# Optimization experiments

Measured on AMD Instinct MI355X. Metric: run time of the kernel, lower is better.

Reference implementation:

```python
import jax, jax.numpy as jnp
import numpy as np
import math

PC_MIN_X, PC_MIN_Y = 0.0, -40.0
VOXEL = 0.05
STRIDE = 8
PE_CH = 16
NEG_SLOPE = 0.01
BN_EPS = 1e-5


def _grid_points():
    # get_pseudo_points: centers of stride-8 BEV cells
    xs = np.arange(0.2, 70.4, 0.4, dtype=np.float32)    # 176
    ys = np.arange(-39.8, 40.2, 0.4, dtype=np.float32)  # 200
    gx, gy = np.meshgrid(xs, ys)                        # (200, 176)
    return jnp.asarray(np.stack([gx, gy], -1).reshape(-1, 2))  # [P, 2]


def _pe3d(D, H, W):
    ch = PE_CH
    div = jnp.exp(jnp.arange(0, ch, 2, dtype=jnp.float32) * (-math.log(10000.0) / ch))
    def enc(n):
        t = jnp.arange(n, dtype=jnp.float32)[:, None] * div[None, :]
        return jnp.concatenate([jnp.sin(t), jnp.cos(t)], axis=-1)  # [n, ch]
    pex = jnp.broadcast_to(enc(D)[:, None, None, :], (D, H, W, ch))
    pey = jnp.broadcast_to(enc(H)[None, :, None, :], (D, H, W, ch))
    pez = jnp.broadcast_to(enc(W)[None, None, :, :], (D, H, W, ch))
    return jnp.concatenate([pex, pey, pez], axis=-1).transpose(3, 0, 1, 2)  # [3*ch, D, H, W]


def _bn_lrelu(h, g, b):
    # eval-mode BatchNorm3d with running_mean=0, running_var=1, then LeakyReLU(0.01)
    h = h * (g / np.sqrt(1.0 + BN_EPS))[None, :, None, None, None] + b[None, :, None, None, None]
    return jnp.where(h >= 0, h, NEG_SLOPE * h)


def _dvf(x, w1, b1, g1, be1, w2, b2, g2, be2, w3, b3):
    N, C, D, H, W = x.shape
    pe = _pe3d(D, H, W)  # [48, D, H, W]
    feats = jnp.concatenate([x, jnp.broadcast_to(pe[None], (N,) + pe.shape)], axis=1)
    h = jnp.einsum('ncdhw,oc->nodhw', feats, w1) + b1[None, :, None, None, None]
    h = _bn_lrelu(h, g1, be1)
    h = jnp.einsum('ncdhw,oc->nodhw', h, w2) + b2[None, :, None, None, None]
    h = _bn_lrelu(h, g2, be2)
    logits = jnp.einsum('ncdhw,oc->nodhw', h, w3) + b3[None, :, None, None, None]  # [N,1,D,H,W]
    wts = jax.nn.softmax(logits, axis=2)  # softmax over depth D
    return (x * wts).reshape(N, C * D, H, W)


def _bilinear(im, x, y):
    # im: (H, W, C), x/y: (P,)  -- faithful to bilinear_interpolate_torch
    H, W = im.shape[0], im.shape[1]
    xf = jnp.floor(x).astype(jnp.int32)
    yf = jnp.floor(y).astype(jnp.int32)
    x0 = jnp.clip(xf, 0, W - 1)
    x1 = jnp.clip(xf + 1, 0, W - 1)
    y0 = jnp.clip(yf, 0, H - 1)
    y1 = jnp.clip(yf + 1, 0, H - 1)
    Ia, Ib, Ic, Id = im[y0, x0], im[y1, x0], im[y0, x1], im[y1, x1]
    x0f, x1f = x0.astype(x.dtype), x1.astype(x.dtype)
    y0f, y1f = y0.astype(y.dtype), y1.astype(y.dtype)
    wa = (x1f - x) * (y1f - y)
    wb = (x1f - x) * (y - y0f)
    wc = (x - x0f) * (y1f - y)
    wd = (x - x0f) * (y - y0f)
    return Ia * wa[:, None] + Ib * wb[:, None] + Ic * wc[:, None] + Id * wd[:, None]


def _rot(p, theta):
    c, s = jnp.cos(theta), jnp.sin(theta)
    return jnp.stack([p[:, 0] * c - p[:, 1] * s, p[:, 0] * s + p[:, 1] * c], axis=-1)


def _bev_align_one(feat, th_prev, th_cur, grid):
    # feat: [C', H, W]; X_TRANS modeled as z-rotation: fwd(current) then inverse(previous)
    Hh, Ww = feat.shape[1], feat.shape[2]
    p = _rot(grid, th_cur)
    p = _rot(p, -th_prev)
    xi = (p[:, 0] - PC_MIN_X) / VOXEL / STRIDE
    yi = (p[:, 1] - PC_MIN_Y) / VOXEL / STRIDE
    out = _bilinear(feat.transpose(1, 2, 0), xi, yi)  # [P, C']
    return out.reshape(Hh, Ww, -1).transpose(2, 0, 1)


def setup_inputs() -> dict:
    key = jax.random.key(0)
    ks = jax.random.split(key, 16)
    N, C, D, H, W = 4, 64, 2, 200, 176
    IN1 = PE_CH * 3 + C  # 112
    inp = {
        'x0': jax.random.normal(ks[0], (N, C, D, H, W), jnp.float32),
        'x1': jax.random.normal(ks[1], (N, C, D, H, W), jnp.float32),
        'transform_param': jax.random.normal(ks[2], (N, 2), jnp.float32) * 0.3,
        'w1': jax.random.normal(ks[3], (C, IN1), jnp.float32) * 0.05,
        'b1': jax.random.normal(ks[4], (C,), jnp.float32) * 0.05,
        'g1': jax.random.uniform(ks[5], (C,), jnp.float32, 0.5, 1.5),
        'be1': jax.random.normal(ks[6], (C,), jnp.float32) * 0.05,
        'w2': jax.random.normal(ks[7], (C // 2, C), jnp.float32) * 0.05,
        'b2': jax.random.normal(ks[8], (C // 2,), jnp.float32) * 0.05,
        'g2': jax.random.uniform(ks[9], (C // 2,), jnp.float32, 0.5, 1.5),
        'be2': jax.random.normal(ks[10], (C // 2,), jnp.float32) * 0.05,
        'w3': jax.random.normal(ks[11], (1, C // 2), jnp.float32) * 0.05,
        'b3': jax.random.normal(ks[12], (1,), jnp.float32) * 0.05,
    }
    return inp


def reference(x0, x1, transform_param, w1, b1, g1, be1, w2, b2, g2, be2, w3, b3):
    mlp = (w1, b1, g1, be1, w2, b2, g2, be2, w3, b3)
    f0 = _dvf(x0, *mlp)  # rot 0: [N, C*D, H, W]
    f1 = _dvf(x1, *mlp)  # rot 1
    grid = _grid_points()
    aligned = jax.vmap(lambda f, tp: _bev_align_one(f, tp[0], tp[1], grid))(f1, transform_param)
    return jnp.maximum(f0, aligned)  # ALIGN_METHOD='max' over stacked feats
```

## Files before the change

kernel.cpp:

```cpp
#include <hip/hip_runtime.h>
#include <hip/hip_bf16.h>
#include <cmath>

#define HW   35200
#define CD   128

typedef short bf16x8 __attribute__((ext_vector_type(8)));
typedef float f32x4  __attribute__((ext_vector_type(4)));

union Frag { unsigned u[4]; bf16x8 v; };

#define OFF_W1B   0
#define OFF_W2B   3072
#define OFF_TD    4096
#define OFF_B2F   4224
#define OFF_W3F   4256
#define OFF_PE    4288
#define OFF_F0B   567488
#define OFF_F1B   9578688

__device__ __forceinline__ float lrelu(float v) { return v >= 0.f ? v : 0.01f * v; }
__device__ __forceinline__ unsigned short f2bf(float f) {
  union { __hip_bfloat16 h; unsigned short u; } c;
  c.h = __float2bfloat16(f);
  return c.u;
}
__device__ __forceinline__ unsigned pack2bf(float lo, float hi) {
  union { __hip_bfloat162 h2; unsigned u; } c;
  c.h2 = __float22bfloat162_rn(float2{lo, hi});
  return c.u;
}
__device__ __forceinline__ float bflo(unsigned u) { return __uint_as_float(u << 16); }
__device__ __forceinline__ float bfhi(unsigned u) { return __uint_as_float(u & 0xffff0000u); }

__global__ void setup_kernel(const float* __restrict__ w1, const float* __restrict__ b1,
                             const float* __restrict__ g1, const float* __restrict__ be1,
                             const float* __restrict__ w2, const float* __restrict__ b2,
                             const float* __restrict__ g2, const float* __restrict__ be2,
                             const float* __restrict__ w3, const float* __restrict__ b3,
                             float* __restrict__ ws) {
  const float RS = rsqrtf(1.0f + 1e-5f);
  unsigned short* w1b = (unsigned short*)(ws + OFF_W1B);
  unsigned short* w2b = (unsigned short*)(ws + OFF_W2B);
  unsigned short* pe  = (unsigned short*)(ws + OFF_PE);
  int i = blockIdx.x * blockDim.x + threadIdx.x;
  if (i < 6144) {
    int e = i & 7, l = (i >> 3) & 63, nt = (i >> 9) & 3, kh = i >> 11;
    int n = nt * 16 + (l & 15);
    int k = kh * 32 + (l >> 4) * 8 + e;
    int col = (kh < 2) ? k : (80 + (k - 64));
    w1b[i] = f2bf(w1[n * 112 + col] * (g1[n] * RS));
    return;
  }
  i -= 6144;
  if (i < 2048) {
    int e = i & 7, l = (i >> 3) & 63, nt = (i >> 9) & 1, kh = i >> 10;
    int n = nt * 16 + (l & 15);
    int k = kh * 32 + (l >> 4) * 8 + e;
    w2b[i] = f2bf(w2[n * 64 + k] * (g2[n] * RS));
    return;
  }
  i -= 2048;
  if (i < 128) {
    int d = i >> 6, o = i & 63;
    float a = 0.f;
    for (int j = 0; j < 8; ++j) {
      float dv = expf((float)(2 * j) * (-0.5756462732485115f));
      float t  = (float)d * dv;
      a += w1[o * 112 + 64 + j] * sinf(t) + w1[o * 112 + 72 + j] * cosf(t);
    }
    ws[OFF_TD + d * 64 + o] = (g1[o] * RS) * (b1[o] + a) + be1[o];
    return;
  }
  i -= 128;
  if (i < 32) { ws[OFF_B2F + i] = b2[i] * (g2[i] * RS) + be2[i]; return; }
  i -= 32;
  if (i < 32) { ws[OFF_W3F + i] = w3[i]; return; }
  i -= 32;
  if (i < 563200) {
    int hw = i >> 4, j = i & 15;
    int h = hw / 176, w = hw - h * 176;
    int jj = j & 7;
    float dv = expf((float)(2 * jj) * (-0.5756462732485115f));
    if (j < 8) {
      float t = (float)h * dv;
      pe[hw * 32 + jj]      = f2bf(sinf(t));
      pe[hw * 32 + 8 + jj]  = f2bf(cosf(t));
    } else {
      float t = (float)w * dv;
      pe[hw * 32 + 16 + jj] = f2bf(sinf(t));
      pe[hw * 32 + 24 + jj] = f2bf(cosf(t));
    }
  }
}

__global__ __launch_bounds__(256)
void mlp_kernel(const float* __restrict__ x0, const float* __restrict__ x1,
                const float* __restrict__ wtab,
                unsigned short* __restrict__ f0b, unsigned short* __restrict__ f1b) {
  __shared__ alignas(16) unsigned short Hs[8 * 128 * 8];

  const int t    = threadIdx.x;
  const int lane = t & 63;
  const int wv   = __builtin_amdgcn_readfirstlane(t >> 6);
  const int g    = lane >> 4;
  const int li   = lane & 15;
  const int n    = blockIdx.y;
  const int inp  = blockIdx.z;
  const int hw0  = blockIdx.x * 64;
  const int pxs  = wv * 16 + li;
  const float* xn = (inp ? x1 : x0) + (size_t)n * CD * HW;
  unsigned short* dst = inp ? f1b : f0b;
  const unsigned short* w1bu = (const unsigned short*)(wtab + OFF_W1B);
  const unsigned short* w2bu = (const unsigned short*)(wtab + OFF_W2B);
  const unsigned short* peg  = (const unsigned short*)(wtab + OFF_PE);

  float xf[2][2][8];
#pragma unroll
  for (int ti = 0; ti < 2; ++ti)
#pragma unroll
    for (int kh = 0; kh < 2; ++kh)
#pragma unroll
      for (int e = 0; e < 8; ++e) {
        const int c = kh * 32 + g * 8 + e;
        xf[ti][kh][e] = xn[(size_t)(c * 2 + ti) * HW + hw0 + pxs];
      }
  const uint4 pev = *(const uint4*)(peg + (size_t)(hw0 + pxs) * 32 + g * 8);

  Frag xb[2][2];
#pragma unroll
  for (int ti = 0; ti < 2; ++ti)
#pragma unroll
    for (int kh = 0; kh < 2; ++kh)
#pragma unroll
      for (int q = 0; q < 4; ++q)
        xb[ti][kh].u[q] = pack2bf(xf[ti][kh][2 * q], xf[ti][kh][2 * q + 1]);
  Frag pf;
  pf.u[0] = pev.x; pf.u[1] = pev.y; pf.u[2] = pev.z; pf.u[3] = pev.w;

  f32x4 acc[2][4];
#pragma unroll
  for (int ti = 0; ti < 2; ++ti)
#pragma unroll
    for (int nt = 0; nt < 4; ++nt) {
      const float tdv = wtab[OFF_TD + ti * 64 + nt * 16 + li];
      acc[ti][nt] = (f32x4){tdv, tdv, tdv, tdv};
    }
#pragma unroll
  for (int kh = 0; kh < 2; ++kh)
#pragma unroll
    for (int nt = 0; nt < 4; ++nt) {
      const bf16x8 b = *(const bf16x8*)&w1bu[(unsigned)((kh * 4 + nt) * 64 + lane) * 8];
      acc[0][nt] = __builtin_amdgcn_mfma_f32_16x16x32_bf16(xb[0][kh].v, b, acc[0][nt], 0, 0, 0);
      acc[1][nt] = __builtin_amdgcn_mfma_f32_16x16x32_bf16(xb[1][kh].v, b, acc[1][nt], 0, 0, 0);
    }
#pragma unroll
  for (int nt = 0; nt < 4; ++nt) {
    const bf16x8 b = *(const bf16x8*)&w1bu[(unsigned)((8 + nt) * 64 + lane) * 8];
    acc[0][nt] = __builtin_amdgcn_mfma_f32_16x16x32_bf16(pf.v, b, acc[0][nt], 0, 0, 0);
    acc[1][nt] = __builtin_amdgcn_mfma_f32_16x16x32_bf16(pf.v, b, acc[1][nt], 0, 0, 0);
  }

#pragma unroll
  for (int ti = 0; ti < 2; ++ti) {
    const int tau = wv + ti * 4;
#pragma unroll
    for (int nt = 0; nt < 4; ++nt)
#pragma unroll
      for (int r = 0; r < 4; ++r) {
        const int o   = nt * 16 + li;
        const int row = tau * 16 + g * 4 + r;
        Hs[(unsigned)((o >> 3) * 128 + row) * 8 + (o & 7)] = f2bf(lrelu(acc[ti][nt][r]));
      }
  }

  f32x4 acc2[2][2];
#pragma unroll
  for (int nt = 0; nt < 2; ++nt) {
    const float bv = wtab[OFF_B2F + nt * 16 + li];
    acc2[0][nt] = (f32x4){bv, bv, bv, bv};
    acc2[1][nt] = acc2[0][nt];
  }
#pragma unroll
  for (int kh = 0; kh < 2; ++kh) {
    const bf16x8 a0 = *(const bf16x8*)&Hs[(unsigned)((kh * 4 + g) * 128 + (wv + 0) * 16 + li) * 8];
    const bf16x8 a1 = *(const bf16x8*)&Hs[(unsigned)((kh * 4 + g) * 128 + (wv + 4) * 16 + li) * 8];
#pragma unroll
    for (int nt = 0; nt < 2; ++nt) {
      const bf16x8 b = *(const bf16x8*)&w2bu[(unsigned)((kh * 2 + nt) * 64 + lane) * 8];
      acc2[0][nt] = __builtin_amdgcn_mfma_f32_16x16x32_bf16(a0, b, acc2[0][nt], 0, 0, 0);
      acc2[1][nt] = __builtin_amdgcn_mfma_f32_16x16x32_bf16(a1, b, acc2[1][nt], 0, 0, 0);
    }
  }

  const float w3a = wtab[OFF_W3F + li];
  const float w3b = wtab[OFF_W3F + 16 + li];
  float wt0[4], wt1[4];
#pragma unroll
  for (int r = 0; r < 4; ++r) {
    float p0 = w3a * lrelu(acc2[0][0][r]) + w3b * lrelu(acc2[0][1][r]);
    float p1 = w3a * lrelu(acc2[1][0][r]) + w3b * lrelu(acc2[1][1][r]);
    p0 += __shfl_xor(p0, 1); p0 += __shfl_xor(p0, 2);
    p0 += __shfl_xor(p0, 4); p0 += __shfl_xor(p0, 8);
    p1 += __shfl_xor(p1, 1); p1 += __shfl_xor(p1, 2);
    p1 += __shfl_xor(p1, 4); p1 += __shfl_xor(p1, 8);
    wt0[r] = 1.f / (1.f + expf(p1 - p0));
    wt1[r] = 1.f / (1.f + expf(p0 - p1));
  }

  const int src = (li >> 2) << 4;
  const float a0 = __shfl(wt0[0], src), b0 = __shfl(wt1[0], src);
  const float a1 = __shfl(wt0[1], src), b1v = __shfl(wt1[1], src);
  const float a2 = __shfl(wt0[2], src), b2v = __shfl(wt1[2], src);
  const float a3 = __shfl(wt0[3], src), b3v = __shfl(wt1[3], src);
  const int r = li & 3;
  const float w0  = (r == 0) ? a0 : (r == 1) ? a1 : (r == 2) ? a2 : a3;
  const float w1v = (r == 0) ? b0 : (r == 1) ? b1v : (r == 2) ? b2v : b3v;

#pragma unroll
  for (int kh = 0; kh < 2; ++kh)
#pragma unroll
    for (int j = 0; j < 4; ++j) {
      const int k = kh * 16 + g * 4 + j;
      const unsigned ua = xb[0][kh].u[j];
      const unsigned ub = xb[1][kh].u[j];
      uint2 pk;
      pk.x = pack2bf(bflo(ua) * w0, bflo(ub) * w1v);
      pk.y = pack2bf(bfhi(ua) * w0, bfhi(ub) * w1v);
      *(uint2*)&dst[(((size_t)n * 32 + k) * HW + hw0 + pxs) * 4] = pk;
    }
}

__global__ __launch_bounds__(256)
void gather_max_kernel(const unsigned short* __restrict__ f0b,
                       const unsigned short* __restrict__ f1b,
                       const float* __restrict__ tp,
                       float* __restrict__ out) {
  const int orig = blockIdx.x;
  const int xcd = orig & 7, idx = orig >> 3;
  const int tile = (xcd < 6 ? xcd * 69 : 6 * 69 + (xcd - 6) * 68) + idx;

  const int tix = threadIdx.x;
  const int px  = tix & 63;
  const int q   = tix >> 6;
  const int n   = blockIdx.y;
  const int hw  = tile * 64 + px;
  const int h   = hw / 176;
  const int w   = hw - h * 176;

  const float thp = tp[n * 2 + 0], thc = tp[n * 2 + 1];
  const float gx = 0.2f + 0.4f * (float)w;
  const float gy = -39.8f + 0.4f * (float)h;
  const float c1 = cosf(thc),  s1v = sinf(thc);
  const float p1x = gx * c1 - gy * s1v;
  const float p1y = gx * s1v + gy * c1;
  const float c2 = cosf(-thp), s2v = sinf(-thp);
  const float p2x = p1x * c2 - p1y * s2v;
  const float p2y = p1x * s2v + p1y * c2;
  const float xi = p2x / 0.05f / 8.f;
  const float yi = (p2y - (-40.f)) / 0.05f / 8.f;

  const float xf = floorf(xi), yf = floorf(yi);
  const int x0i = (int)xf, y0i = (int)yf;
  const int x0c = min(max(x0i,     0), 175);
  const int x1c = min(max(x0i + 1, 0), 175);
  const int y0c = min(max(y0i,     0), 199);
  const int y1c = min(max(y0i + 1, 0), 199);
  const float x0f = (float)x0c, x1f = (float)x1c;
  const float y0f = (float)y0c, y1f = (float)y1c;
  const float wa = (x1f - xi) * (y1f - yi);
  const float wb = (x1f - xi) * (yi - y0f);
  const float wc = (xi - x0f) * (y1f - yi);
  const float wd = (xi - x0f) * (yi - y0f);
  const int ta = y0c * 176 + x0c, tb = y1c * 176 + x0c;
  const int tc = y0c * 176 + x1c, td = y1c * 176 + x1c;

#pragma unroll
  for (int i = 0; i < 8; ++i) {
    const int k = q * 8 + i;
    const int cd0 = k * 4;
    const unsigned short* fp1 = f1b + ((size_t)n * 32 + k) * HW * 4;
    const uint2 Ia = *(const uint2*)(fp1 + (size_t)ta * 4);
    const uint2 Ib = *(const uint2*)(fp1 + (size_t)tb * 4);
    const uint2 Ic = *(const uint2*)(fp1 + (size_t)tc * 4);
    const uint2 Id = *(const uint2*)(fp1 + (size_t)td * 4);
    float4 sv;
    sv.x = bflo(Ia.x) * wa + bflo(Ib.x) * wb + bflo(Ic.x) * wc + bflo(Id.x) * wd;
    sv.y = bfhi(Ia.x) * wa + bfhi(Ib.x) * wb + bfhi(Ic.x) * wc + bfhi(Id.x) * wd;
    sv.z = bflo(Ia.y) * wa + bflo(Ib.y) * wb + bflo(Ic.y) * wc + bflo(Id.y) * wd;
    sv.w = bfhi(Ia.y) * wa + bfhi(Ib.y) * wb + bfhi(Ic.y) * wc + bfhi(Id.y) * wd;

    const uint2 F0 = *(const uint2*)(f0b + (((size_t)n * 32 + k) * HW + hw) * 4);

    float* op = out + ((size_t)n * CD + cd0) * HW + hw;
    op[0]              = fmaxf(bflo(F0.x), sv.x);
    op[HW]             = fmaxf(bfhi(F0.x), sv.y);
    op[2 * (size_t)HW] = fmaxf(bflo(F0.y), sv.z);
    op[3 * (size_t)HW] = fmaxf(bfhi(F0.y), sv.w);
  }
}

extern "C" void kernel_launch(void* const* d_in, const int* in_sizes, int n_in,
                              void* d_out, int out_size, void* d_ws, size_t ws_size,
                              hipStream_t stream) {
  const float* x0  = (const float*)d_in[0];
  const float* x1  = (const float*)d_in[1];
  const float* tp  = (const float*)d_in[2];
  const float* w1  = (const float*)d_in[3];
  const float* b1  = (const float*)d_in[4];
  const float* g1  = (const float*)d_in[5];
  const float* be1 = (const float*)d_in[6];
  const float* w2  = (const float*)d_in[7];
  const float* b2  = (const float*)d_in[8];
  const float* g2  = (const float*)d_in[9];
  const float* be2 = (const float*)d_in[10];
  const float* w3  = (const float*)d_in[11];
  const float* b3  = (const float*)d_in[12];
  float* ws = (float*)d_ws;
  unsigned short* f0b = (unsigned short*)(ws + OFF_F0B);
  unsigned short* f1b = (unsigned short*)(ws + OFF_F1B);

  setup_kernel<<<2233, 256, 0, stream>>>(w1, b1, g1, be1, w2, b2, g2, be2, w3, b3, ws);

  dim3 g1d(550, 4, 2);
  mlp_kernel<<<g1d, 256, 0, stream>>>(x0, x1, ws, f0b, f1b);

  dim3 g2d(550, 4);
  gather_max_kernel<<<g2d, 256, 0, stream>>>(f0b, f1b, tp, (float*)d_out);
}
```

Measured before the change: 93.01 us.

## Process two adjacent pixels per lane in MLP kernel with wider loads/stores

The MLP kernel now uses 128 threads per block, with each lane handling two adjacent pixels. Input loads become float2, the positional-encoding loads are doubled, and output stores become 16-byte uint4 writes. MFMA work per wave doubles to keep the same pixels per block. The aim is to cut the number of memory instructions and improve coalescing width, at the cost of higher register pressure and fewer waves per block.

After: 98.64 us. 6.1% more time.

```diff
diff --git a/kernel.cpp b/kernel.cpp
--- a/kernel.cpp
+++ b/kernel.cpp
@@ -94,7 +94,7 @@
   }
 }
 
-__global__ __launch_bounds__(256)
+__global__ __launch_bounds__(128)
 void mlp_kernel(const float* __restrict__ x0, const float* __restrict__ x1,
                 const float* __restrict__ wtab,
                 unsigned short* __restrict__ f0b, unsigned short* __restrict__ f1b) {
@@ -102,132 +102,163 @@
 
   const int t    = threadIdx.x;
   const int lane = t & 63;
-  const int wv   = __builtin_amdgcn_readfirstlane(t >> 6);
+  const int w    = __builtin_amdgcn_readfirstlane(t >> 6);
   const int g    = lane >> 4;
   const int li   = lane & 15;
   const int n    = blockIdx.y;
   const int inp  = blockIdx.z;
   const int hw0  = blockIdx.x * 64;
-  const int pxs  = wv * 16 + li;
+  const int pxl  = 32 * w + 2 * li;
+  const int pxe  = hw0 + pxl;
   const float* xn = (inp ? x1 : x0) + (size_t)n * CD * HW;
   unsigned short* dst = inp ? f1b : f0b;
   const unsigned short* w1bu = (const unsigned short*)(wtab + OFF_W1B);
   const unsigned short* w2bu = (const unsigned short*)(wtab + OFF_W2B);
   const unsigned short* peg  = (const unsigned short*)(wtab + OFF_PE);
 
-  float xf[2][2][8];
-#pragma unroll
-  for (int ti = 0; ti < 2; ++ti)
+  float2 xf2[2][2][8];
+#pragma unroll
+  for (int d = 0; d < 2; ++d)
 #pragma unroll
     for (int kh = 0; kh < 2; ++kh)
 #pragma unroll
       for (int e = 0; e < 8; ++e) {
         const int c = kh * 32 + g * 8 + e;
-        xf[ti][kh][e] = xn[(size_t)(c * 2 + ti) * HW + hw0 + pxs];
+        xf2[d][kh][e] = *(const float2*)&xn[(size_t)(c * 2 + d) * HW + pxe];
       }
-  const uint4 pev = *(const uint4*)(peg + (size_t)(hw0 + pxs) * 32 + g * 8);
-
-  Frag xb[2][2];
-#pragma unroll
-  for (int ti = 0; ti < 2; ++ti)
+  const uint4 pev0 = *(const uint4*)(peg + (size_t)pxe * 32 + g * 8);
+  const uint4 pev1 = *(const uint4*)(peg + (size_t)(pxe + 1) * 32 + g * 8);
+
+  Frag xb[2][2][2];
+#pragma unroll
+  for (int d = 0; d < 2; ++d)
 #pragma unroll
     for (int kh = 0; kh < 2; ++kh)
 #pragma unroll
-      for (int q = 0; q < 4; ++q)
-        xb[ti][kh].u[q] = pack2bf(xf[ti][kh][2 * q], xf[ti][kh][2 * q + 1]);
-  Frag pf;
-  pf.u[0] = pev.x; pf.u[1] = pev.y; pf.u[2] = pev.z; pf.u[3] = pev.w;
-
-  f32x4 acc[2][4];
-#pragma unroll
-  for (int ti = 0; ti < 2; ++ti)
+      for (int q = 0; q < 4; ++q) {
+        xb[0][d][kh].u[q] = pack2bf(xf2[d][kh][2 * q].x, xf2[d][kh][2 * q + 1].x);
+        xb[1][d][kh].u[q] = pack2bf(xf2[d][kh][2 * q].y, xf2[d][kh][2 * q + 1].y);
+      }
+  Frag pf[2];
+  pf[0].u[0] = pev0.x; pf[0].u[1] = pev0.y; pf[0].u[2] = pev0.z; pf[0].u[3] = pev0.w;
+  pf[1].u[0] = pev1.x; pf[1].u[1] = pev1.y; pf[1].u[2] = pev1.z; pf[1].u[3] = pev1.w;
+
+  f32x4 acc[2][2][4];
+#pragma unroll
+  for (int d = 0; d < 2; ++d)
 #pragma unroll
     for (int nt = 0; nt < 4; ++nt) {
-      const float tdv = wtab[OFF_TD + ti * 64 + nt * 16 + li];
-      acc[ti][nt] = (f32x4){tdv, tdv, tdv, tdv};
+      const float tdv = wtab[OFF_TD + d * 64 + nt * 16 + li];
+      acc[0][d][nt] = (f32x4){tdv, tdv, tdv, tdv};
+      acc[1][d][nt] = acc[0][d][nt];
     }
 #pragma unroll
   for (int kh = 0; kh < 2; ++kh)
 #pragma unroll
     for (int nt = 0; nt < 4; ++nt) {
       const bf16x8 b = *(const bf16x8*)&w1bu[(unsigned)((kh * 4 + nt) * 64 + lane) * 8];
-      acc[0][nt] = __builtin_amdgcn_mfma_f32_16x16x32_bf16(xb[0][kh].v, b, acc[0][nt], 0, 0, 0);
-      acc[1][nt] = __builtin_amdgcn_mfma_f32_16x16x32_bf16(xb[1][kh].v, b, acc[1][nt], 0, 0, 0);
+#pragma unroll
+      for (int pxt = 0; pxt < 2; ++pxt)
+#pragma unroll
+        for (int d = 0; d < 2; ++d)
+          acc[pxt][d][nt] = __builtin_amdgcn_mfma_f32_16x16x32_bf16(xb[pxt][d][kh].v, b, acc[pxt][d][nt], 0, 0, 0);
     }
 #pragma unroll
   for (int nt = 0; nt < 4; ++nt) {
     const bf16x8 b = *(const bf16x8*)&w1bu[(unsigned)((8 + nt) * 64 + lane) * 8];
-    acc[0][nt] = __builtin_amdgcn_mfma_f32_16x16x32_bf16(pf.v, b, acc[0][nt], 0, 0, 0);
-    acc[1][nt] = __builtin_amdgcn_mfma_f32_16x16x32_bf16(pf.v, b, acc[1][nt], 0, 0, 0);
-  }
-
-#pragma unroll
-  for (int ti = 0; ti < 2; ++ti) {
-    const int tau = wv + ti * 4;
-#pragma unroll
-    for (int nt = 0; nt < 4; ++nt)
-#pragma unroll
-      for (int r = 0; r < 4; ++r) {
-        const int o   = nt * 16 + li;
-        const int row = tau * 16 + g * 4 + r;
-        Hs[(unsigned)((o >> 3) * 128 + row) * 8 + (o & 7)] = f2bf(lrelu(acc[ti][nt][r]));
-      }
-  }
-
-  f32x4 acc2[2][2];
+#pragma unroll
+    for (int pxt = 0; pxt < 2; ++pxt)
+#pragma unroll
+      for (int d = 0; d < 2; ++d)
+        acc[pxt][d][nt] = __builtin_amdgcn_mfma_f32_16x16x32_bf16(pf[pxt].v, b, acc[pxt][d][nt], 0, 0, 0);
+  }
+
+#pragma unroll
+  for (int pxt = 0; pxt < 2; ++pxt)
+#pragma unroll
+    for (int d = 0; d < 2; ++d)
+#pragma unroll
+      for (int nt = 0; nt < 4; ++nt)
+#pragma unroll
+        for (int r = 0; r < 4; ++r) {
+          const int o    = nt * 16 + li;
+          const int rowl = d * 64 + 32 * w + 2 * (g * 4 + r) + pxt;
+          Hs[(unsigned)((o >> 3) * 128 + rowl) * 8 + (o & 7)] = f2bf(lrelu(acc[pxt][d][nt][r]));
+        }
+
+  f32x4 acc2[2][2][2];
 #pragma unroll
   for (int nt = 0; nt < 2; ++nt) {
     const float bv = wtab[OFF_B2F + nt * 16 + li];
-    acc2[0][nt] = (f32x4){bv, bv, bv, bv};
-    acc2[1][nt] = acc2[0][nt];
+    acc2[0][0][nt] = (f32x4){bv, bv, bv, bv};
+    acc2[0][1][nt] = acc2[0][0][nt];
+    acc2[1][0][nt] = acc2[0][0][nt];
+    acc2[1][1][nt] = acc2[0][0][nt];
   }
 #pragma unroll
   for (int kh = 0; kh < 2; ++kh) {
-    const bf16x8 a0 = *(const bf16x8*)&Hs[(unsigned)((kh * 4 + g) * 128 + (wv + 0) * 16 + li) * 8];
-    const bf16x8 a1 = *(const bf16x8*)&Hs[(unsigned)((kh * 4 + g) * 128 + (wv + 4) * 16 + li) * 8];
+    bf16x8 a[2][2];
+#pragma unroll
+    for (int pxt = 0; pxt < 2; ++pxt)
+#pragma unroll
+      for (int d = 0; d < 2; ++d)
+        a[pxt][d] = *(const bf16x8*)&Hs[(unsigned)((kh * 4 + g) * 128 + d * 64 + 32 * w + 2 * li + pxt) * 8];
 #pragma unroll
     for (int nt = 0; nt < 2; ++nt) {
       const bf16x8 b = *(const bf16x8*)&w2bu[(unsigned)((kh * 2 + nt) * 64 + lane) * 8];
-      acc2[0][nt] = __builtin_amdgcn_mfma_f32_16x16x32_bf16(a0, b, acc2[0][nt], 0, 0, 0);
-      acc2[1][nt] = __builtin_amdgcn_mfma_f32_16x16x32_bf16(a1, b, acc2[1][nt], 0, 0, 0);
+#pragma unroll
+      for (int pxt = 0; pxt < 2; ++pxt)
+#pragma unroll
+        for (int d = 0; d < 2; ++d)
+          acc2[pxt][d][nt] = __builtin_amdgcn_mfma_f32_16x16x32_bf16(a[pxt][d], b, acc2[pxt][d][nt], 0, 0, 0);
     }
   }
 
   const float w3a = wtab[OFF_W3F + li];
   const float w3b = wtab[OFF_W3F + 16 + li];
-  float wt0[4], wt1[4];
+  float wtv[2][2][4];
+#pragma unroll
+  for (int pxt = 0; pxt < 2; ++pxt)
+#pragma unroll
+    for (int r = 0; r < 4; ++r) {
+      float p0 = w3a * lrelu(acc2[pxt][0][0][r]) + w3b * lrelu(acc2[pxt][0][1][r]);
+      float p1 = w3a * lrelu(acc2[pxt][1][0][r]) + w3b * lrelu(acc2[pxt][1][1][r]);
+      p0 += __shfl_xor(p0, 1); p0 += __shfl_xor(p0, 2);
+      p0 += __shfl_xor(p0, 4); p0 += __shfl_xor(p0, 8);
+      p1 += __shfl_xor(p1, 1); p1 += __shfl_xor(p1, 2);
+      p1 += __shfl_xor(p1, 4); p1 += __shfl_xor(p1, 8);
+      wtv[pxt][0][r] = 1.f / (1.f + expf(p1 - p0));
+      wtv[pxt][1][r] = 1.f / (1.f + expf(p0 - p1));
+    }
+
+  const int src = (li >> 2) << 4;
+  float ae[4], be[4], ao[4], bo[4];
 #pragma unroll
   for (int r = 0; r < 4; ++r) {
-    float p0 = w3a * lrelu(acc2[0][0][r]) + w3b * lrelu(acc2[0][1][r]);
-    float p1 = w3a * lrelu(acc2[1][0][r]) + w3b * lrelu(acc2[1][1][r]);
-    p0 += __shfl_xor(p0, 1); p0 += __shfl_xor(p0, 2);
-    p0 += __shfl_xor(p0, 4); p0 += __shfl_xor(p0, 8);
-    p1 += __shfl_xor(p1, 1); p1 += __shfl_xor(p1, 2);
-    p1 += __shfl_xor(p1, 4); p1 += __shfl_xor(p1, 8);
-    wt0[r] = 1.f / (1.f + expf(p1 - p0));
-    wt1[r] = 1.f / (1.f + expf(p0 - p1));
-  }
-
-  const int src = (li >> 2) << 4;
-  const float a0 = __shfl(wt0[0], src), b0 = __shfl(wt1[0], src);
-  const float a1 = __shfl(wt0[1], src), b1v = __shfl(wt1[1], src);
-  const float a2 = __shfl(wt0[2], src), b2v = __shfl(wt1[2], src);
-  const float a3 = __shfl(wt0[3], src), b3v = __shfl(wt1[3], src);
-  const int r = li & 3;
-  const float w0  = (r == 0) ? a0 : (r == 1) ? a1 : (r == 2) ? a2 : a3;
-  const float w1v = (r == 0) ? b0 : (r == 1) ? b1v : (r == 2) ? b2v : b3v;
+    ae[r] = __shfl(wtv[0][0][r], src); be[r] = __shfl(wtv[0][1][r], src);
+    ao[r] = __shfl(wtv[1][0][r], src); bo[r] = __shfl(wtv[1][1][r], src);
+  }
+  const int rs = li & 3;
+  const float w0e = (rs == 0) ? ae[0] : (rs == 1) ? ae[1] : (rs == 2) ? ae[2] : ae[3];
+  const float w1e = (rs == 0) ? be[0] : (rs == 1) ? be[1] : (rs == 2) ? be[2] : be[3];
+  const float w0o = (rs == 0) ? ao[0] : (rs == 1) ? ao[1] : (rs == 2) ? ao[2] : ao[3];
+  const float w1o = (rs == 0) ? bo[0] : (rs == 1) ? bo[1] : (rs == 2) ? bo[2] : bo[3];
 
 #pragma unroll
   for (int kh = 0; kh < 2; ++kh)
 #pragma unroll
     for (int j = 0; j < 4; ++j) {
       const int k = kh * 16 + g * 4 + j;
-      const unsigned ua = xb[0][kh].u[j];
-      const unsigned ub = xb[1][kh].u[j];
-      uint2 pk;
-      pk.x = pack2bf(bflo(ua) * w0, bflo(ub) * w1v);
-      pk.y = pack2bf(bfhi(ua) * w0, bfhi(ub) * w1v);
-      *(uint2*)&dst[(((size_t)n * 32 + k) * HW + hw0 + pxs) * 4] = pk;
+      const unsigned ua0 = xb[0][0][kh].u[j];
+      const unsigned ub0 = xb[0][1][kh].u[j];
+      const unsigned ua1 = xb[1][0][kh].u[j];
+      const unsigned ub1 = xb[1][1][kh].u[j];
+      uint4 pk;
+      pk.x = pack2bf(bflo(ua0) * w0e, bflo(ub0) * w1e);
+      pk.y = pack2bf(bfhi(ua0) * w0e, bfhi(ub0) * w1e);
+      pk.z = pack2bf(bflo(ua1) * w0o, bflo(ub1) * w1o);
+      pk.w = pack2bf(bfhi(ua1) * w0o, bfhi(ub1) * w1o);
+      *(uint4*)&dst[(((size_t)n * 32 + k) * HW + pxe) * 4] = pk;
     }
 }
 
@@ -323,7 +354,7 @@
   setup_kernel<<<2233, 256, 0, stream>>>(w1, b1, g1, be1, w2, b2, g2, be2, w3, b3, ws);
 
   dim3 g1d(550, 4, 2);
-  mlp_kernel<<<g1d, 256, 0, stream>>>(x0, x1, ws, f0b, f1b);
+  mlp_kernel<<<g1d, 128, 0, stream>>>(x0, x1, ws, f0b, f1b);
 
   dim3 g2d(550, 4);
   gather_max_kernel<<<g2d, 256, 0, stream>>>(f0b, f1b, tp, (float*)d_out);
```
